# Kernel optimization log

Hardware: AMD Instinct MI355X
Metric: run time of the kernel (lower is better)

Reference implementation:

```python
import jax, jax.numpy as jnp
import numpy as np

B, N, H, L = 8, 256, 128, 3
NF, EF, TD, FH = 6, 15, 4, 64  # node feat, edge feat, temporal dim, flow hidden


def setup_inputs() -> dict:
    key = jax.random.key(0)
    ks = jax.random.split(key, 16)
    s = 0.05
    return {
        "node_features": jax.random.normal(ks[0], (B, N, NF), jnp.float32),
        "edge_features": jax.random.normal(ks[1], (B, N, N, EF), jnp.float32),
        "temporal_features": jax.random.normal(ks[2], (B, N, N, TD), jnp.float32),
        "adjacency": jax.random.randint(ks[3], (N, N), 0, 2, jnp.int32),
        "W_emb": jax.random.normal(ks[4], (NF, H), jnp.float32) * s,
        "b_emb": jnp.zeros((H,), jnp.float32),
        "msg_W": jax.random.normal(ks[5], (L, H + 3, H), jnp.float32) * s,
        "msg_b": jnp.zeros((L, H), jnp.float32),
        "upd_W": jax.random.normal(ks[6], (L, 2 * H, H), jnp.float32) * s,
        "upd_b": jnp.zeros((L, H), jnp.float32),
        "W1": jax.random.normal(ks[7], (2 * H + 3 + TD, FH), jnp.float32) * s,
        "b1": jnp.zeros((FH,), jnp.float32),
        "W2": jax.random.normal(ks[8], (FH, 1), jnp.float32) * s,
        "b2": jnp.zeros((1,), jnp.float32),
    }


def reference(node_features, edge_features, temporal_features, adjacency,
              W_emb, b_emb, msg_W, msg_b, upd_W, upd_b, W1, b1, W2, b2):
    # mask[j, i] = 1 if node i is a neighbor of node j (adjacency[j] > 0)
    mask = (adjacency > 0).astype(node_features.dtype)          # [N, N]
    deg = mask.sum(axis=1)                                      # [N]
    edge_rel = edge_features[..., -3:]                          # [B, N, N, 3]
    # aggregated relation features per destination j: sum_i mask[j,i] * edge_rel[b,i,j,:]
    r_agg = jnp.einsum('ji,bijc->bjc', mask, edge_rel)          # [B, N, 3]

    # node embedding (dropout = identity in eval)
    emb = jax.nn.relu(node_features @ W_emb + b_emb)            # [B, N, H]

    for l in range(L):
        We, Wr = msg_W[l, :H], msg_W[l, H:]                     # [H,H], [3,H]
        # msg_nn is linear, so the masked sum decomposes exactly:
        # messages[b,j] = sum_i mask[j,i]*(emb_i @ We + r_ij @ Wr + b)
        messages = (jnp.einsum('ji,bih->bjh', mask, emb @ We)
                    + r_agg @ Wr
                    + deg[None, :, None] * msg_b[l])            # [B, N, H]
        emb = jax.nn.relu(
            jnp.concatenate([emb, messages], axis=-1) @ upd_W[l] + upd_b[l])

    # pairwise flow MLP, first Linear split by input blocks [emb_i, emb_j, r, t]
    Wi, Wj = W1[:H], W1[H:2 * H]
    Wr1, Wt = W1[2 * H:2 * H + 3], W1[2 * H + 3:]
    hi = emb @ Wi                                               # [B, N, FH]
    hj = emb @ Wj                                               # [B, N, FH]
    h = jax.nn.relu(hi[:, :, None, :] + hj[:, None, :, :]
                    + edge_rel @ Wr1 + temporal_features @ Wt + b1)  # [B,N,N,FH]
    flows = jax.nn.relu(h @ W2 + b2)[..., 0]                    # [B, N, N]
    return flows
```

## Files before the change

### kernel.cpp

```cpp
#include <hip/hip_runtime.h>

#define B 8
#define N 256
#define H 128
#define NF 6
#define EF 15
#define TD 4
#define FH 64
#define M (B*N)

typedef unsigned short u16;
using short8  = __attribute__((ext_vector_type(8))) short;
using short4v = __attribute__((ext_vector_type(4))) short;
using f32x4   = __attribute__((ext_vector_type(4))) float;

__device__ __forceinline__ u16 f2bf(float x) {
    unsigned u = __float_as_uint(x);
    u += 0x7fffu + ((u >> 16) & 1u);
    return (u16)(u >> 16);
}
__device__ __forceinline__ float bf2f(u16 h) {
    return __uint_as_float(((unsigned)h) << 16);
}

__global__ __launch_bounds__(256) void k_setup(
    const float* __restrict__ edge, const int* __restrict__ adj,
    const float* __restrict__ nf, const float* __restrict__ Wemb,
    const float* __restrict__ bemb,
    const float* __restrict__ msg_W, const float* __restrict__ upd_W,
    const float* __restrict__ W1,
    float* __restrict__ e0p, float* __restrict__ e1p, float* __restrict__ e2p,
    float* __restrict__ rp0, float* __restrict__ rp1, float* __restrict__ rp2,
    float* __restrict__ deg,
    u16* __restrict__ WeTh, u16* __restrict__ WeTl,
    u16* __restrict__ UwTh, u16* __restrict__ UwTl,
    u16* __restrict__ W1Th, u16* __restrict__ W1Tl,
    u16* __restrict__ eRh, u16* __restrict__ eRl,
    u16* __restrict__ eTh, u16* __restrict__ eTl)
{
    __shared__ __align__(16) float smem[3848];
    __shared__ float red[4];
    const int t = threadIdx.x;
    const int blk = blockIdx.x;

    if (blk < 2048) {
        const int i = blk & 255;
        const float* src = edge + (size_t)blk * (N * EF);
        float4* s4 = (float4*)smem;
#pragma unroll
        for (int u = 0; u < 4; ++u) {
            int idx = t + u * 256;
            if (idx < (N * EF) / 4) s4[idx] = *(const float4*)(src + idx * 4);
        }
        __syncthreads();
        const int j = t;
        float e0 = smem[j * EF + 12];
        float e1 = smem[j * EF + 13];
        float e2 = smem[j * EF + 14];
        size_t base = (size_t)blk * N + j;
        e0p[base] = e0; e1p[base] = e1; e2p[base] = e2;
        float m = (adj[j * N + i] > 0) ? 1.f : 0.f;
        rp0[base] = m * e0; rp1[base] = m * e1; rp2[base] = m * e2;
    } else if (blk < 2688) {
        int idx = (blk - 2048) * 256 + t;
        float v; u16 *dh, *dl; int d;
        if (idx < 3 * 16384) {
            int l = idx / 16384, r = idx & 16383;
            int c = r >> 7, h = r & 127;
            v = msg_W[l * ((H + 3) * H) + h * H + c];
            dh = WeTh; dl = WeTl; d = idx;
        } else if (idx < 3 * 16384 + 3 * 32768) {
            int r0 = idx - 3 * 16384;
            int l = r0 / 32768, r = r0 & 32767;
            int c = r >> 8, k = r & 255;
            v = upd_W[l * (2 * H * H) + k * H + c];
            dh = UwTh; dl = UwTl; d = r0;
        } else {
            int r0 = idx - 3 * 16384 - 3 * 32768;
            int f = r0 >> 8, k = r0 & 255;
            v = W1[k * FH + f];
            dh = W1Th; dl = W1Tl; d = r0;
        }
        u16 h = f2bf(v);
        dh[d] = h;
        dl[d] = f2bf(v - bf2f(h));
    } else if (blk < 2816) {
        int tile = blk - 2688;
        float (*sout)[132] = (float(*)[132])smem;
        {
            int row = t >> 4, h0 = (t & 15) * 8;
            int gr = tile * 16 + row;
            float xv[NF];
#pragma unroll
            for (int k = 0; k < NF; ++k) xv[k] = nf[gr * NF + k];
#pragma unroll
            for (int c = 0; c < 8; ++c) {
                float a = bemb[h0 + c];
#pragma unroll
                for (int k = 0; k < NF; ++k) a += xv[k] * Wemb[k * H + h0 + c];
                sout[row][h0 + c] = fmaxf(a, 0.f);
            }
        }
        __syncthreads();
        {
            int row = t >> 4, h0 = (t & 15) * 8;
            int gr = tile * 16 + row;
            short8 ph, pl;
#pragma unroll
            for (int c = 0; c < 8; ++c) {
                float x = sout[row][h0 + c];
                u16 h = f2bf(x);
                ph[c] = (short)h;
                pl[c] = (short)f2bf(x - bf2f(h));
            }
            *(short8*)&eRh[(size_t)gr * H + h0] = ph;
            *(short8*)&eRl[(size_t)gr * H + h0] = pl;
        }
        {
            int hh = t >> 1, jj = (t & 1) * 8;
            short8 th, tl;
#pragma unroll
            for (int r = 0; r < 8; ++r) {
                float x = sout[jj + r][hh];
                u16 h = f2bf(x);
                th[r] = (short)h;
                tl[r] = (short)f2bf(x - bf2f(h));
            }
            size_t o = (size_t)(tile >> 4) * H * N + (size_t)hh * N + ((tile & 15) * 16) + jj;
            *(short8*)&eTh[o] = th;
            *(short8*)&eTl[o] = tl;
        }
    } else {
        int jr = blk - 2816;
        float v = (adj[jr * N + t] > 0) ? 1.f : 0.f;
        for (int o = 32; o > 0; o >>= 1) v += __shfl_down(v, o);
        if ((t & 63) == 0) red[t >> 6] = v;
        __syncthreads();
        if (t == 0) deg[jr] = red[0] + red[1] + red[2] + red[3];
    }
}

#define PIPE(NC, LD, COMP)                          \
    LD(0, pA0, pA1);                                \
    LD(1, pB0, pB1);                                \
    WRX(0, pA0, pA1);                               \
    __syncthreads();                                \
    _Pragma("unroll")                               \
    for (int c = 0; c < (NC); c += 2) {             \
        WRX(1, pB0, pB1);                           \
        if (c + 2 < (NC)) LD(c + 2, pA0, pA1);      \
        COMP(c, 0);                                 \
        __syncthreads();                            \
        if (c + 2 < (NC)) WRX(0, pA0, pA1);         \
        if (c + 3 < (NC)) LD(c + 3, pB0, pB1);      \
        COMP(c + 1, 1);                             \
        __syncthreads();                            \
    }

template <bool FIRST, bool LAST>
__global__ __launch_bounds__(512) void k_layer(
    const u16* __restrict__ embR_hi, const u16* __restrict__ embR_lo,
    const u16* __restrict__ embT_hi, const u16* __restrict__ embT_lo,
    const int* __restrict__ adj,
    const float* __restrict__ rp0, const float* __restrict__ rp1,
    const float* __restrict__ rp2, float* __restrict__ ragg,
    const float* __restrict__ deg,
    const u16* __restrict__ WeT_hi, const u16* __restrict__ WeT_lo,
    const float* __restrict__ mwl, const float* __restrict__ mbl,
    const u16* __restrict__ UwT_hi, const u16* __restrict__ UwT_lo,
    const float* __restrict__ ubl,
    u16* __restrict__ oR_hi, u16* __restrict__ oR_lo,
    u16* __restrict__ oT_hi, u16* __restrict__ oT_lo,
    const u16* __restrict__ W1T_hi, const u16* __restrict__ W1T_lo,
    float* __restrict__ hi_out, float* __restrict__ hj_out)
{
    __shared__ __align__(16) u16 sbt[2][2][128][40];
    __shared__ __align__(16) u16 smask[16][264];
    __shared__ __align__(16) u16 semb_hi[16][136], semb_lo[16][136];
    __shared__ __align__(16) u16 sagg_hi[16][136], sagg_lo[16][136];
    __shared__ __align__(16) u16 smsg_hi[16][136], smsg_lo[16][136];
    __shared__ __align__(16) float sout[16][132];
    __shared__ float sragg[16][4];

    const int t = threadIdx.x;
    const int wave = t >> 6, lane = t & 63;
    const int lrow = lane & 15;
    const int kg8  = (lane >> 4) * 8;
    const int rb   = (lane >> 4) * 4;
    const int cb   = wave * 16;
    const int blk  = blockIdx.x;
    const int b    = blk >> 4, tile = blk & 15;
    const int j0   = tile * 16;
    const int gb   = b * N;

    const int sp = t >> 8, task = t & 255;
    const int sh = task >> 2, sseg = (task & 3) * 8;

    short8 pA0, pA1, pB0, pB1;

    {
        int j = t >> 5, i0 = (t & 31) * 8;
        int4 a0 = *(const int4*)(adj + (j0 + j) * N + i0);
        int4 a1 = *(const int4*)(adj + (j0 + j) * N + i0 + 4);
        short8 mrow;
        mrow[0] = (a0.x > 0) ? (short)0x3F80 : (short)0;
        mrow[1] = (a0.y > 0) ? (short)0x3F80 : (short)0;
        mrow[2] = (a0.z > 0) ? (short)0x3F80 : (short)0;
        mrow[3] = (a0.w > 0) ? (short)0x3F80 : (short)0;
        mrow[4] = (a1.x > 0) ? (short)0x3F80 : (short)0;
        mrow[5] = (a1.y > 0) ? (short)0x3F80 : (short)0;
        mrow[6] = (a1.z > 0) ? (short)0x3F80 : (short)0;
        mrow[7] = (a1.w > 0) ? (short)0x3F80 : (short)0;
        *(short8*)&smask[j][i0] = mrow;
        int h0 = (t & 31) * 4;
        *(short4v*)&semb_hi[j][h0] = *(const short4v*)&embR_hi[(size_t)(gb + j0 + j) * H + h0];
        *(short4v*)&semb_lo[j][h0] = *(const short4v*)&embR_lo[(size_t)(gb + j0 + j) * H + h0];
    }

    if constexpr (FIRST) {
        int j16 = t >> 5, ic = t & 31;
        int gj = gb + j0 + j16;
        float s0 = 0.f, s1 = 0.f, s2 = 0.f;
#pragma unroll
        for (int k = 0; k < 8; ++k) {
            size_t o = ((size_t)(gb + ic * 8 + k)) * N + (j0 + j16);
            s0 += rp0[o]; s1 += rp1[o]; s2 += rp2[o];
        }
        for (int o = 16; o > 0; o >>= 1) {
            s0 += __shfl_down(s0, o, 32);
            s1 += __shfl_down(s1, o, 32);
            s2 += __shfl_down(s2, o, 32);
        }
        if (ic == 0) {
            sragg[j16][0] = s0; sragg[j16][1] = s1; sragg[j16][2] = s2;
            float* rg = ragg + (size_t)gj * 3;
            rg[0] = s0; rg[1] = s1; rg[2] = s2;
        }
    } else {
        if (t < 48) sragg[t / 3][t % 3] = ragg[(size_t)(gb + j0 + t / 3) * 3 + (t % 3)];
    }

    const u16* sA_hi = embT_hi + (size_t)b * H * N;
    const u16* sA_lo = embT_lo + (size_t)b * H * N;

#define WRX(buf, q0, q1)                              \
    { *(short8*)&sbt[buf][sp][sh][sseg] = q0;         \
      *(short8*)&sbt[buf][sp][sh + 64][sseg] = q1; }

#define LDA(c, q0, q1)                                                        \
    { const u16* s_ = sp ? sA_lo : sA_hi;                                     \
      q0 = *(const short8*)(s_ + (size_t)sh * N + (c) * 32 + sseg);           \
      q1 = *(const short8*)(s_ + (size_t)(sh + 64) * N + (c) * 32 + sseg); }

#define LDB(c, q0, q1)                                                        \
    { const u16* s_ = sp ? WeT_lo : WeT_hi;                                   \
      q0 = *(const short8*)(s_ + (size_t)sh * H + (c) * 32 + sseg);           \
      q1 = *(const short8*)(s_ + (size_t)(sh + 64) * H + (c) * 32 + sseg); }

#define LDC(c, q0, q1)                                                        \
    { const u16* s_ = sp ? UwT_lo : UwT_hi;                                   \
      q0 = *(const short8*)(s_ + (size_t)sh * 2 * H + (c) * 32 + sseg);       \
      q1 = *(const short8*)(s_ + (size_t)(sh + 64) * 2 * H + (c) * 32 + sseg); }

#define LDD(c, q0, q1)                                                        \
    { const u16* s_ = sp ? W1T_lo : W1T_hi;                                   \
      q0 = *(const short8*)(s_ + (size_t)sh * 256 + (c) * 32 + sseg);         \
      q1 = *(const short8*)(s_ + (size_t)sh * 256 + 128 + (c) * 32 + sseg); }

#define COMPA(c, buf)                                                           \
    { short8 am = *(const short8*)&smask[lrow][(c) * 32 + kg8];                 \
      short8 bh = *(const short8*)&sbt[buf][0][cb + lrow][kg8];                 \
      short8 bl = *(const short8*)&sbt[buf][1][cb + lrow][kg8];                 \
      acc = __builtin_amdgcn_mfma_f32_16x16x32_bf16(am, bh, acc, 0, 0, 0);      \
      acc = __builtin_amdgcn_mfma_f32_16x16x32_bf16(am, bl, acc, 0, 0, 0); }

#define COMPB(c, buf)                                                           \
    { short8 ah = *(const short8*)&sagg_hi[lrow][(c) * 32 + kg8];               \
      short8 al = *(const short8*)&sagg_lo[lrow][(c) * 32 + kg8];               \
      short8 bh = *(const short8*)&sbt[buf][0][cb + lrow][kg8];                 \
      short8 bl = *(const short8*)&sbt[buf][1][cb + lrow][kg8];                 \
      acc = __builtin_amdgcn_mfma_f32_16x16x32_bf16(ah, bh, acc, 0, 0, 0);      \
      acc = __builtin_amdgcn_mfma_f32_16x16x32_bf16(ah, bl, acc, 0, 0, 0);      \
      acc = __builtin_amdgcn_mfma_f32_16x16x32_bf16(al, bh, acc, 0, 0, 0); }

#define COMPC(c, buf)                                                           \
    { int kc = ((c) & 3) * 32 + kg8; short8 ah, al;                             \
      if ((c) < 4) { ah = *(const short8*)&semb_hi[lrow][kc];                   \
                     al = *(const short8*)&semb_lo[lrow][kc]; }                 \
      else         { ah = *(const short8*)&smsg_hi[lrow][kc];                   \
                     al = *(const short8*)&smsg_lo[lrow][kc]; }                 \
      short8 bh = *(const short8*)&sbt[buf][0][cb + lrow][kg8];                 \
      short8 bl = *(const short8*)&sbt[buf][1][cb + lrow][kg8];                 \
      acc = __builtin_amdgcn_mfma_f32_16x16x32_bf16(ah, bh, acc, 0, 0, 0);      \
      acc = __builtin_amdgcn_mfma_f32_16x16x32_bf16(ah, bl, acc, 0, 0, 0);      \
      acc = __builtin_amdgcn_mfma_f32_16x16x32_bf16(al, bh, acc, 0, 0, 0); }

#define COMPD(c, buf)                                                           \
    { short8 ah = *(const short8*)&sagg_hi[lrow][(c) * 32 + kg8];               \
      short8 al = *(const short8*)&sagg_lo[lrow][(c) * 32 + kg8];               \
      short8 bh = *(const short8*)&sbt[buf][0][br][kg8];                        \
      short8 bl = *(const short8*)&sbt[buf][1][br][kg8];                        \
      acc = __builtin_amdgcn_mfma_f32_16x16x32_bf16(ah, bh, acc, 0, 0, 0);      \
      acc = __builtin_amdgcn_mfma_f32_16x16x32_bf16(ah, bl, acc, 0, 0, 0);      \
      acc = __builtin_amdgcn_mfma_f32_16x16x32_bf16(al, bh, acc, 0, 0, 0); }

    f32x4 acc = {0.f, 0.f, 0.f, 0.f};
    PIPE(8, LDA, COMPA)
#pragma unroll
    for (int r = 0; r < 4; ++r) {
        float v = acc[r];
        u16 h = f2bf(v);
        sagg_hi[rb + r][cb + lrow] = h;
        sagg_lo[rb + r][cb + lrow] = f2bf(v - bf2f(h));
    }

    acc = (f32x4){0.f, 0.f, 0.f, 0.f};
    PIPE(4, LDB, COMPB)
    {
        int hp = cb + lrow;
        float w0 = mwl[(H + 0) * H + hp];
        float w1 = mwl[(H + 1) * H + hp];
        float w2 = mwl[(H + 2) * H + hp];
        float mb = mbl[hp];
#pragma unroll
        for (int r = 0; r < 4; ++r) {
            int jl = j0 + rb + r;
            float v = acc[r] + deg[jl] * mb
                    + sragg[rb + r][0] * w0 + sragg[rb + r][1] * w1
                    + sragg[rb + r][2] * w2;
            u16 h = f2bf(v);
            smsg_hi[rb + r][hp] = h;
            smsg_lo[rb + r][hp] = f2bf(v - bf2f(h));
        }
    }

    acc = (f32x4){0.f, 0.f, 0.f, 0.f};
    PIPE(8, LDC, COMPC)
    {
        float ub = ubl[cb + lrow];
#pragma unroll
        for (int r = 0; r < 4; ++r) {
            float v = fmaxf(acc[r] + ub, 0.f);
            if constexpr (LAST) {
                u16 h = f2bf(v);
                sagg_hi[rb + r][cb + lrow] = h;
                sagg_lo[rb + r][cb + lrow] = f2bf(v - bf2f(h));
            } else {
                sout[rb + r][cb + lrow] = v;
            }
        }
    }
    __syncthreads();

    if constexpr (!LAST) {
        {
            int row = t >> 5, h0 = (t & 31) * 4;
            int gr = gb + j0 + row;
            float4 v = *(const float4*)&sout[row][h0];
            float xs[4] = {v.x, v.y, v.z, v.w};
            short4v ph, pl;
#pragma unroll
            for (int c = 0; c < 4; ++c) {
                u16 h = f2bf(xs[c]);
                ph[c] = (short)h;
                pl[c] = (short)f2bf(xs[c] - bf2f(h));
            }
            *(short4v*)&oR_hi[(size_t)gr * H + h0] = ph;
            *(short4v*)&oR_lo[(size_t)gr * H + h0] = pl;
        }
        {
            int hh = t >> 2, jj = (t & 3) * 4;
            short4v th, tl;
#pragma unroll
            for (int r = 0; r < 4; ++r) {
                float x = sout[jj + r][hh];
                u16 h = f2bf(x);
                th[r] = (short)h;
                tl[r] = (short)f2bf(x - bf2f(h));
            }
            size_t o = (size_t)b * H * N + (size_t)hh * N + j0 + jj;
            *(short4v*)&oT_hi[o] = th;
            *(short4v*)&oT_lo[o] = tl;
        }
    } else {
        const int br = ((wave >= 4) ? 64 : 0) + (wave & 3) * 16 + lrow;
        acc = (f32x4){0.f, 0.f, 0.f, 0.f};
        PIPE(4, LDD, COMPD)
#pragma unroll
        for (int r = 0; r < 4; ++r) sout[rb + r][br] = acc[r];
        __syncthreads();
        int row = t >> 5, c0 = (t & 31) * 4;
        int gr = gb + j0 + row;
        float4 v = *(const float4*)&sout[row][c0];
        if (c0 < 64) *(float4*)&hi_out[(size_t)gr * FH + c0] = v;
        else         *(float4*)&hj_out[(size_t)gr * FH + (c0 - 64)] = v;
    }
#undef WRX
#undef LDA
#undef LDB
#undef LDC
#undef LDD
#undef COMPA
#undef COMPB
#undef COMPC
#undef COMPD
}

__global__ __launch_bounds__(256) void k_final(
    const float* __restrict__ hi, const float* __restrict__ hj,
    const float* __restrict__ e0p, const float* __restrict__ e1p,
    const float* __restrict__ e2p, const float* __restrict__ temporal,
    const float* __restrict__ W1, const float* __restrict__ b1,
    const float* __restrict__ W2, const float* __restrict__ b2,
    float* __restrict__ flows) {
    __shared__ float his[8][FH];
    __shared__ float hjs[32][FH + 2];
    __shared__ float wr0[FH], wr1[FH], wr2[FH];
    __shared__ float wt0[FH], wt1[FH], wt2[FH], wt3[FH], bb[FH], w2s[FH];
    int blk = blockIdx.x;
    int jt = blk & 7, it = (blk >> 3) & 31, b = blk >> 8;
    int tid = threadIdx.x;
#pragma unroll
    for (int u = 0; u < 2; ++u) {
        int idx = u * 256 + tid;
        his[idx >> 6][idx & 63] = hi[((size_t)(b * N) + it * 8 + (idx >> 6)) * FH + (idx & 63)];
    }
#pragma unroll
    for (int u = 0; u < 8; ++u) {
        int idx = u * 256 + tid;
        hjs[idx >> 6][idx & 63] = hj[((size_t)(b * N) + jt * 32 + (idx >> 6)) * FH + (idx & 63)];
    }
    {
        int f = tid & 63, g = tid >> 6;
        if (g == 0) { wr0[f] = W1[(2 * H + 0) * FH + f]; wt0[f] = W1[(2 * H + 3) * FH + f]; bb[f] = b1[f]; }
        if (g == 1) { wr1[f] = W1[(2 * H + 1) * FH + f]; wt1[f] = W1[(2 * H + 4) * FH + f]; w2s[f] = W2[f]; }
        if (g == 2) { wr2[f] = W1[(2 * H + 2) * FH + f]; wt2[f] = W1[(2 * H + 5) * FH + f]; }
        if (g == 3) { wt3[f] = W1[(2 * H + 6) * FH + f]; }
    }
    __syncthreads();
    int ti = tid >> 5, tj = tid & 31;
    int i = it * 8 + ti, j = jt * 32 + tj;
    size_t pij = ((size_t)(b * N) + i) * N + j;
    float e0 = e0p[pij], e1 = e1p[pij], e2 = e2p[pij];
    float4 tf = *(const float4*)(temporal + pij * TD);
    float acc = 0.f;
#pragma unroll 8
    for (int f = 0; f < FH; ++f) {
        float v = his[ti][f] + hjs[tj][f] + bb[f]
                + e0 * wr0[f] + e1 * wr1[f] + e2 * wr2[f]
                + tf.x * wt0[f] + tf.y * wt1[f] + tf.z * wt2[f] + tf.w * wt3[f];
        acc += fmaxf(v, 0.f) * w2s[f];
    }
    flows[pij] = fmaxf(acc + b2[0], 0.f);
}

extern "C" void kernel_launch(void* const* d_in, const int* in_sizes, int n_in,
                              void* d_out, int out_size, void* d_ws, size_t ws_size,
                              hipStream_t stream) {
    const float* nf       = (const float*)d_in[0];
    const float* edge     = (const float*)d_in[1];
    const float* temporal = (const float*)d_in[2];
    const int*   adj      = (const int*)d_in[3];
    const float* W_emb    = (const float*)d_in[4];
    const float* b_emb    = (const float*)d_in[5];
    const float* msg_W    = (const float*)d_in[6];
    const float* msg_b    = (const float*)d_in[7];
    const float* upd_W    = (const float*)d_in[8];
    const float* upd_b    = (const float*)d_in[9];
    const float* W1       = (const float*)d_in[10];
    const float* b1       = (const float*)d_in[11];
    const float* W2       = (const float*)d_in[12];
    const float* b2       = (const float*)d_in[13];
    float* out = (float*)d_out;
    (void)in_sizes; (void)n_in; (void)out_size; (void)ws_size;

    char* p = (char*)d_ws;
    auto take = [&](size_t bytes) { char* r = p; p += (bytes + 255) & ~(size_t)255; return r; };
    float* deg   = (float*)take(256 * 4);
    float* ragg  = (float*)take((size_t)M * 3 * 4);
    float* e0p   = (float*)take((size_t)B * N * N * 4);
    float* e1p   = (float*)take((size_t)B * N * N * 4);
    float* e2p   = (float*)take((size_t)B * N * N * 4);
    float* rp0   = (float*)take((size_t)B * N * N * 4);
    float* rp1   = (float*)take((size_t)B * N * N * 4);
    float* rp2   = (float*)take((size_t)B * N * N * 4);
    float* hi    = (float*)take((size_t)M * FH * 4);
    float* hj    = (float*)take((size_t)M * FH * 4);
    u16* eRhA = (u16*)take((size_t)M * H * 2);
    u16* eRlA = (u16*)take((size_t)M * H * 2);
    u16* eThA = (u16*)take((size_t)M * H * 2);
    u16* eTlA = (u16*)take((size_t)M * H * 2);
    u16* eRhB = (u16*)take((size_t)M * H * 2);
    u16* eRlB = (u16*)take((size_t)M * H * 2);
    u16* eThB = (u16*)take((size_t)M * H * 2);
    u16* eTlB = (u16*)take((size_t)M * H * 2);
    u16* WeTh = (u16*)take(3 * 16384 * 2);
    u16* WeTl = (u16*)take(3 * 16384 * 2);
    u16* UwTh = (u16*)take(3 * 32768 * 2);
    u16* UwTl = (u16*)take(3 * 32768 * 2);
    u16* W1Th = (u16*)take(16384 * 2);
    u16* W1Tl = (u16*)take(16384 * 2);

    k_setup<<<3072, 256, 0, stream>>>(edge, adj, nf, W_emb, b_emb,
                                      msg_W, upd_W, W1,
                                      e0p, e1p, e2p, rp0, rp1, rp2, deg,
                                      WeTh, WeTl, UwTh, UwTl, W1Th, W1Tl,
                                      eRhA, eRlA, eThA, eTlA);

    const int mwS = (H + 3) * H;
    k_layer<true, false><<<128, 512, 0, stream>>>(
        eRhA, eRlA, eThA, eTlA, adj, rp0, rp1, rp2, ragg, deg,
        WeTh + 0 * 16384, WeTl + 0 * 16384, msg_W + 0 * mwS, msg_b + 0 * H,
        UwTh + 0 * 32768, UwTl + 0 * 32768, upd_b + 0 * H,
        eRhB, eRlB, eThB, eTlB, W1Th, W1Tl, hi, hj);
    k_layer<false, false><<<128, 512, 0, stream>>>(
        eRhB, eRlB, eThB, eTlB, adj, rp0, rp1, rp2, ragg, deg,
        WeTh + 1 * 16384, WeTl + 1 * 16384, msg_W + 1 * mwS, msg_b + 1 * H,
        UwTh + 1 * 32768, UwTl + 1 * 32768, upd_b + 1 * H,
        eRhA, eRlA, eThA, eTlA, W1Th, W1Tl, hi, hj);
    k_layer<false, true><<<128, 512, 0, stream>>>(
        eRhA, eRlA, eThA, eTlA, adj, rp0, rp1, rp2, ragg, deg,
        WeTh + 2 * 16384, WeTl + 2 * 16384, msg_W + 2 * mwS, msg_b + 2 * H,
        UwTh + 2 * 32768, UwTl + 2 * 32768, upd_b + 2 * H,
        eRhB, eRlB, eThB, eTlB, W1Th, W1Tl, hi, hj);

    k_final<<<2048, 256, 0, stream>>>(hi, hj, e0p, e1p, e2p, temporal,
                                      W1, b1, W2, b2, out);
}
```

Baseline: 73.78 us.

## Fuse setup, layers and flow MLP into one cooperative persistent kernel

Replaces the five separate launches (setup, three GNN layers, final flow MLP) with a single cooperative kernel of 256 blocks that separates the phases with grid-wide syncs and overlays their shared memory in a union. The setup phase is rebalanced so each block streams eight edge rows with double-buffered loads, and the final phase loops over four j-tiles per block. The aim is to remove launch gaps and tail effects between short kernels. In exchange, only 128 of 256 blocks do work in the layer phases, grid syncs add their own cost, and occupancy is bounded by the union's shared memory size.

```diff
diff --git a/kernel.cpp b/kernel.cpp
--- a/kernel.cpp
+++ b/kernel.cpp
@@ -1,4 +1,7 @@
 #include <hip/hip_runtime.h>
+#include <hip/hip_cooperative_groups.h>
+
+namespace cg = cooperative_groups;
 
 #define B 8
 #define N 256
@@ -23,121 +26,59 @@
     return __uint_as_float(((unsigned)h) << 16);
 }
 
-__global__ __launch_bounds__(256) void k_setup(
-    const float* __restrict__ edge, const int* __restrict__ adj,
-    const float* __restrict__ nf, const float* __restrict__ Wemb,
-    const float* __restrict__ bemb,
-    const float* __restrict__ msg_W, const float* __restrict__ upd_W,
-    const float* __restrict__ W1,
-    float* __restrict__ e0p, float* __restrict__ e1p, float* __restrict__ e2p,
-    float* __restrict__ rp0, float* __restrict__ rp1, float* __restrict__ rp2,
-    float* __restrict__ deg,
-    u16* __restrict__ WeTh, u16* __restrict__ WeTl,
-    u16* __restrict__ UwTh, u16* __restrict__ UwTl,
-    u16* __restrict__ W1Th, u16* __restrict__ W1Tl,
-    u16* __restrict__ eRh, u16* __restrict__ eRl,
-    u16* __restrict__ eTh, u16* __restrict__ eTl)
-{
-    __shared__ __align__(16) float smem[3848];
-    __shared__ float red[4];
-    const int t = threadIdx.x;
-    const int blk = blockIdx.x;
-
-    if (blk < 2048) {
-        const int i = blk & 255;
-        const float* src = edge + (size_t)blk * (N * EF);
-        float4* s4 = (float4*)smem;
-#pragma unroll
-        for (int u = 0; u < 4; ++u) {
-            int idx = t + u * 256;
-            if (idx < (N * EF) / 4) s4[idx] = *(const float4*)(src + idx * 4);
-        }
-        __syncthreads();
-        const int j = t;
-        float e0 = smem[j * EF + 12];
-        float e1 = smem[j * EF + 13];
-        float e2 = smem[j * EF + 14];
-        size_t base = (size_t)blk * N + j;
-        e0p[base] = e0; e1p[base] = e1; e2p[base] = e2;
-        float m = (adj[j * N + i] > 0) ? 1.f : 0.f;
-        rp0[base] = m * e0; rp1[base] = m * e1; rp2[base] = m * e2;
-    } else if (blk < 2688) {
-        int idx = (blk - 2048) * 256 + t;
-        float v; u16 *dh, *dl; int d;
-        if (idx < 3 * 16384) {
-            int l = idx / 16384, r = idx & 16383;
-            int c = r >> 7, h = r & 127;
-            v = msg_W[l * ((H + 3) * H) + h * H + c];
-            dh = WeTh; dl = WeTl; d = idx;
-        } else if (idx < 3 * 16384 + 3 * 32768) {
-            int r0 = idx - 3 * 16384;
-            int l = r0 / 32768, r = r0 & 32767;
-            int c = r >> 8, k = r & 255;
-            v = upd_W[l * (2 * H * H) + k * H + c];
-            dh = UwTh; dl = UwTl; d = r0;
-        } else {
-            int r0 = idx - 3 * 16384 - 3 * 32768;
-            int f = r0 >> 8, k = r0 & 255;
-            v = W1[k * FH + f];
-            dh = W1Th; dl = W1Tl; d = r0;
-        }
-        u16 h = f2bf(v);
-        dh[d] = h;
-        dl[d] = f2bf(v - bf2f(h));
-    } else if (blk < 2816) {
-        int tile = blk - 2688;
-        float (*sout)[132] = (float(*)[132])smem;
-        {
-            int row = t >> 4, h0 = (t & 15) * 8;
-            int gr = tile * 16 + row;
-            float xv[NF];
-#pragma unroll
-            for (int k = 0; k < NF; ++k) xv[k] = nf[gr * NF + k];
-#pragma unroll
-            for (int c = 0; c < 8; ++c) {
-                float a = bemb[h0 + c];
-#pragma unroll
-                for (int k = 0; k < NF; ++k) a += xv[k] * Wemb[k * H + h0 + c];
-                sout[row][h0 + c] = fmaxf(a, 0.f);
-            }
-        }
-        __syncthreads();
-        {
-            int row = t >> 4, h0 = (t & 15) * 8;
-            int gr = tile * 16 + row;
-            short8 ph, pl;
-#pragma unroll
-            for (int c = 0; c < 8; ++c) {
-                float x = sout[row][h0 + c];
-                u16 h = f2bf(x);
-                ph[c] = (short)h;
-                pl[c] = (short)f2bf(x - bf2f(h));
-            }
-            *(short8*)&eRh[(size_t)gr * H + h0] = ph;
-            *(short8*)&eRl[(size_t)gr * H + h0] = pl;
-        }
-        {
-            int hh = t >> 1, jj = (t & 1) * 8;
-            short8 th, tl;
-#pragma unroll
-            for (int r = 0; r < 8; ++r) {
-                float x = sout[jj + r][hh];
-                u16 h = f2bf(x);
-                th[r] = (short)h;
-                tl[r] = (short)f2bf(x - bf2f(h));
-            }
-            size_t o = (size_t)(tile >> 4) * H * N + (size_t)hh * N + ((tile & 15) * 16) + jj;
-            *(short8*)&eTh[o] = th;
-            *(short8*)&eTl[o] = tl;
-        }
+struct LayerSM {
+    u16 sbt[2][2][128][40];
+    u16 smask[16][264];
+    u16 semb_hi[16][136], semb_lo[16][136];
+    u16 sagg_hi[16][136], sagg_lo[16][136];
+    u16 smsg_hi[16][136], smsg_lo[16][136];
+    float sout[16][132];
+    float sragg[16][4];
+};
+struct SetupSM {
+    float edge[2][3840];
+    float sout[16][132];
+    float red[8];
+};
+struct FinalSM {
+    float his[8][FH];
+    float hjs[64][FH + 3];
+    float wr[3][FH], wt[4][FH], bb[FH], w2s[FH];
+};
+union SMu { LayerSM L; SetupSM S; FinalSM F; };
+
+struct Params {
+    const float* edge; const float* temporal; const int* adj;
+    const float* nf; const float* Wemb; const float* bemb;
+    const float* msgW; const float* msgb; const float* updW; const float* updb;
+    const float* W1; const float* b1; const float* W2; const float* b2;
+    float *e0p, *e1p, *e2p, *rp0, *rp1, *rp2, *deg, *ragg, *hi, *hj, *out;
+    u16 *eRhA, *eRlA, *eThA, *eTlA, *eRhB, *eRlB, *eThB, *eTlB;
+    u16 *WeTh, *WeTl, *UwTh, *UwTl, *W1Th, *W1Tl;
+};
+
+__device__ __forceinline__ void wtrans(int idx, const Params& p) {
+    float v; u16 *dh, *dl; int d;
+    if (idx < 3 * 16384) {
+        int l = idx / 16384, r = idx & 16383;
+        int c = r >> 7, h = r & 127;
+        v = p.msgW[l * ((H + 3) * H) + h * H + c];
+        dh = p.WeTh; dl = p.WeTl; d = idx;
+    } else if (idx < 3 * 16384 + 3 * 32768) {
+        int r0 = idx - 3 * 16384;
+        int l = r0 / 32768, r = r0 & 32767;
+        int c = r >> 8, k = r & 255;
+        v = p.updW[l * (2 * H * H) + k * H + c];
+        dh = p.UwTh; dl = p.UwTl; d = r0;
     } else {
-        int jr = blk - 2816;
-        float v = (adj[jr * N + t] > 0) ? 1.f : 0.f;
-        for (int o = 32; o > 0; o >>= 1) v += __shfl_down(v, o);
-        if ((t & 63) == 0) red[t >> 6] = v;
-        __syncthreads();
-        if (t == 0) deg[jr] = red[0] + red[1] + red[2] + red[3];
-    }
+        int r0 = idx - 3 * 16384 - 3 * 32768;
+        int f = r0 >> 8, k = r0 & 255;
+        v = p.W1[k * FH + f];
+        dh = p.W1Th; dl = p.W1Tl; d = r0;
+    }
+    u16 h = f2bf(v);
+    dh[d] = h;
+    dl[d] = f2bf(v - bf2f(h));
 }
 
 #define PIPE(NC, LD, COMP)                          \
@@ -158,41 +99,28 @@
     }
 
 template <bool FIRST, bool LAST>
-__global__ __launch_bounds__(512) void k_layer(
-    const u16* __restrict__ embR_hi, const u16* __restrict__ embR_lo,
-    const u16* __restrict__ embT_hi, const u16* __restrict__ embT_lo,
-    const int* __restrict__ adj,
-    const float* __restrict__ rp0, const float* __restrict__ rp1,
-    const float* __restrict__ rp2, float* __restrict__ ragg,
-    const float* __restrict__ deg,
-    const u16* __restrict__ WeT_hi, const u16* __restrict__ WeT_lo,
-    const float* __restrict__ mwl, const float* __restrict__ mbl,
-    const u16* __restrict__ UwT_hi, const u16* __restrict__ UwT_lo,
-    const float* __restrict__ ubl,
-    u16* __restrict__ oR_hi, u16* __restrict__ oR_lo,
-    u16* __restrict__ oT_hi, u16* __restrict__ oT_lo,
-    const u16* __restrict__ W1T_hi, const u16* __restrict__ W1T_lo,
-    float* __restrict__ hi_out, float* __restrict__ hj_out)
+__device__ void layer_body(SMu& sm, const Params& p, int blk, int t,
+    const u16* embR_hi, const u16* embR_lo,
+    const u16* embT_hi, const u16* embT_lo,
+    const u16* WeT_hi, const u16* WeT_lo,
+    const float* mwl, const float* mbl,
+    const u16* UwT_hi, const u16* UwT_lo, const float* ubl,
+    u16* oR_hi, u16* oR_lo, u16* oT_hi, u16* oT_lo)
 {
-    __shared__ __align__(16) u16 sbt[2][2][128][40];
-    __shared__ __align__(16) u16 smask[16][264];
-    __shared__ __align__(16) u16 semb_hi[16][136], semb_lo[16][136];
-    __shared__ __align__(16) u16 sagg_hi[16][136], sagg_lo[16][136];
-    __shared__ __align__(16) u16 smsg_hi[16][136], smsg_lo[16][136];
-    __shared__ __align__(16) float sout[16][132];
-    __shared__ float sragg[16][4];
-
-    const int t = threadIdx.x;
+    auto& sbt = sm.L.sbt;       auto& smask = sm.L.smask;
+    auto& semb_hi = sm.L.semb_hi; auto& semb_lo = sm.L.semb_lo;
+    auto& sagg_hi = sm.L.sagg_hi; auto& sagg_lo = sm.L.sagg_lo;
+    auto& smsg_hi = sm.L.smsg_hi; auto& smsg_lo = sm.L.smsg_lo;
+    auto& sout = sm.L.sout;     auto& sragg = sm.L.sragg;
+
     const int wave = t >> 6, lane = t & 63;
     const int lrow = lane & 15;
     const int kg8  = (lane >> 4) * 8;
     const int rb   = (lane >> 4) * 4;
     const int cb   = wave * 16;
-    const int blk  = blockIdx.x;
     const int b    = blk >> 4, tile = blk & 15;
     const int j0   = tile * 16;
     const int gb   = b * N;
-
     const int sp = t >> 8, task = t & 255;
     const int sh = task >> 2, sseg = (task & 3) * 8;
 
@@ -200,8 +128,8 @@
 
     {
         int j = t >> 5, i0 = (t & 31) * 8;
-        int4 a0 = *(const int4*)(adj + (j0 + j) * N + i0);
-        int4 a1 = *(const int4*)(adj + (j0 + j) * N + i0 + 4);
+        int4 a0 = *(const int4*)(p.adj + (j0 + j) * N + i0);
+        int4 a1 = *(const int4*)(p.adj + (j0 + j) * N + i0 + 4);
         short8 mrow;
         mrow[0] = (a0.x > 0) ? (short)0x3F80 : (short)0;
         mrow[1] = (a0.y > 0) ? (short)0x3F80 : (short)0;
@@ -224,7 +152,7 @@
 #pragma unroll
         for (int k = 0; k < 8; ++k) {
             size_t o = ((size_t)(gb + ic * 8 + k)) * N + (j0 + j16);
-            s0 += rp0[o]; s1 += rp1[o]; s2 += rp2[o];
+            s0 += p.rp0[o]; s1 += p.rp1[o]; s2 += p.rp2[o];
         }
         for (int o = 16; o > 0; o >>= 1) {
             s0 += __shfl_down(s0, o, 32);
@@ -233,11 +161,11 @@
         }
         if (ic == 0) {
             sragg[j16][0] = s0; sragg[j16][1] = s1; sragg[j16][2] = s2;
-            float* rg = ragg + (size_t)gj * 3;
+            float* rg = p.ragg + (size_t)gj * 3;
             rg[0] = s0; rg[1] = s1; rg[2] = s2;
         }
     } else {
-        if (t < 48) sragg[t / 3][t % 3] = ragg[(size_t)(gb + j0 + t / 3) * 3 + (t % 3)];
+        if (t < 48) sragg[t / 3][t % 3] = p.ragg[(size_t)(gb + j0 + t / 3) * 3 + (t % 3)];
     }
 
     const u16* sA_hi = embT_hi + (size_t)b * H * N;
@@ -263,7 +191,7 @@
       q1 = *(const short8*)(s_ + (size_t)(sh + 64) * 2 * H + (c) * 32 + sseg); }
 
 #define LDD(c, q0, q1)                                                        \
-    { const u16* s_ = sp ? W1T_lo : W1T_hi;                                   \
+    { const u16* s_ = sp ? p.W1Tl : p.W1Th;                                   \
       q0 = *(const short8*)(s_ + (size_t)sh * 256 + (c) * 32 + sseg);         \
       q1 = *(const short8*)(s_ + (size_t)sh * 256 + 128 + (c) * 32 + sseg); }
 
@@ -325,7 +253,7 @@
 #pragma unroll
         for (int r = 0; r < 4; ++r) {
             int jl = j0 + rb + r;
-            float v = acc[r] + deg[jl] * mb
+            float v = acc[r] + p.deg[jl] * mb
                     + sragg[rb + r][0] * w0 + sragg[rb + r][1] * w1
                     + sragg[rb + r][2] * w2;
             u16 h = f2bf(v);
@@ -392,8 +320,8 @@
         int row = t >> 5, c0 = (t & 31) * 4;
         int gr = gb + j0 + row;
         float4 v = *(const float4*)&sout[row][c0];
-        if (c0 < 64) *(float4*)&hi_out[(size_t)gr * FH + c0] = v;
-        else         *(float4*)&hj_out[(size_t)gr * FH + (c0 - 64)] = v;
+        if (c0 < 64) *(float4*)&p.hi[(size_t)gr * FH + c0] = v;
+        else         *(float4*)&p.hj[(size_t)gr * FH + (c0 - 64)] = v;
     }
 #undef WRX
 #undef LDA
@@ -406,124 +334,221 @@
 #undef COMPD
 }
 
-__global__ __launch_bounds__(256) void k_final(
-    const float* __restrict__ hi, const float* __restrict__ hj,
-    const float* __restrict__ e0p, const float* __restrict__ e1p,
-    const float* __restrict__ e2p, const float* __restrict__ temporal,
-    const float* __restrict__ W1, const float* __restrict__ b1,
-    const float* __restrict__ W2, const float* __restrict__ b2,
-    float* __restrict__ flows) {
-    __shared__ float his[8][FH];
-    __shared__ float hjs[32][FH + 2];
-    __shared__ float wr0[FH], wr1[FH], wr2[FH];
-    __shared__ float wt0[FH], wt1[FH], wt2[FH], wt3[FH], bb[FH], w2s[FH];
-    int blk = blockIdx.x;
-    int jt = blk & 7, it = (blk >> 3) & 31, b = blk >> 8;
-    int tid = threadIdx.x;
-#pragma unroll
-    for (int u = 0; u < 2; ++u) {
-        int idx = u * 256 + tid;
-        his[idx >> 6][idx & 63] = hi[((size_t)(b * N) + it * 8 + (idx >> 6)) * FH + (idx & 63)];
-    }
-#pragma unroll
-    for (int u = 0; u < 8; ++u) {
-        int idx = u * 256 + tid;
-        hjs[idx >> 6][idx & 63] = hj[((size_t)(b * N) + jt * 32 + (idx >> 6)) * FH + (idx & 63)];
-    }
+__global__ __launch_bounds__(512, 2) void k_mega(Params p) {
+    cg::grid_group grid = cg::this_grid();
+    __shared__ SMu sm;
+    const int blk = blockIdx.x;
+    const int t = threadIdx.x;
+
     {
-        int f = tid & 63, g = tid >> 6;
-        if (g == 0) { wr0[f] = W1[(2 * H + 0) * FH + f]; wt0[f] = W1[(2 * H + 3) * FH + f]; bb[f] = b1[f]; }
-        if (g == 1) { wr1[f] = W1[(2 * H + 1) * FH + f]; wt1[f] = W1[(2 * H + 4) * FH + f]; w2s[f] = W2[f]; }
-        if (g == 2) { wr2[f] = W1[(2 * H + 2) * FH + f]; wt2[f] = W1[(2 * H + 5) * FH + f]; }
-        if (g == 3) { wt3[f] = W1[(2 * H + 6) * FH + f]; }
-    }
-    __syncthreads();
-    int ti = tid >> 5, tj = tid & 31;
-    int i = it * 8 + ti, j = jt * 32 + tj;
-    size_t pij = ((size_t)(b * N) + i) * N + j;
-    float e0 = e0p[pij], e1 = e1p[pij], e2 = e2p[pij];
-    float4 tf = *(const float4*)(temporal + pij * TD);
-    float acc = 0.f;
+        const int b = blk >> 5, ic = blk & 31;
+        float4 r0, r1;
+        auto loadTask = [&](int k) {
+            const float* src = p.edge + ((size_t)(b * N + ic * 8 + k)) * (N * EF);
+            r0 = *(const float4*)(src + t * 4);
+            if (t < 448) r1 = *(const float4*)(src + t * 4 + 2048);
+        };
+        auto writeTask = [&](int buf) {
+            *(float4*)&sm.S.edge[buf][t * 4] = r0;
+            if (t < 448) *(float4*)&sm.S.edge[buf][t * 4 + 2048] = r1;
+        };
+        loadTask(0);
+        writeTask(0);
+        for (int k = 0; k < 8; ++k) {
+            __syncthreads();
+            if (k < 7) loadTask(k + 1);
+            {
+                const int i = ic * 8 + k;
+                const int j = t & 255;
+                const float* eb = sm.S.edge[k & 1];
+                float e0 = eb[j * EF + 12];
+                float e1 = eb[j * EF + 13];
+                float e2 = eb[j * EF + 14];
+                size_t base = ((size_t)(b * N + i)) * N + j;
+                if (t < 256) {
+                    p.e0p[base] = e0; p.e1p[base] = e1; p.e2p[base] = e2;
+                } else {
+                    float m = (p.adj[j * N + i] > 0) ? 1.f : 0.f;
+                    p.rp0[base] = m * e0; p.rp1[base] = m * e1; p.rp2[base] = m * e2;
+                }
+            }
+            if (k < 7) writeTask((k + 1) & 1);
+        }
+        __syncthreads();
+
+        wtrans(blk * 512 + t, p);
+        if (blk < 64) wtrans(131072 + blk * 512 + t, p);
+
+        if (blk < 128) {
+            const int tile = blk;
+            int row = t >> 5, h0 = (t & 31) * 4;
+            int gr = tile * 16 + row;
+            float xv[NF];
+#pragma unroll
+            for (int k = 0; k < NF; ++k) xv[k] = p.nf[gr * NF + k];
+#pragma unroll
+            for (int c = 0; c < 4; ++c) {
+                float a = p.bemb[h0 + c];
+#pragma unroll
+                for (int k = 0; k < NF; ++k) a += xv[k] * p.Wemb[k * H + h0 + c];
+                sm.S.sout[row][h0 + c] = fmaxf(a, 0.f);
+            }
+            __syncthreads();
+            {
+                short4v ph, pl;
+#pragma unroll
+                for (int c = 0; c < 4; ++c) {
+                    float x = sm.S.sout[row][h0 + c];
+                    u16 h = f2bf(x);
+                    ph[c] = (short)h;
+                    pl[c] = (short)f2bf(x - bf2f(h));
+                }
+                *(short4v*)&p.eRhA[(size_t)gr * H + h0] = ph;
+                *(short4v*)&p.eRlA[(size_t)gr * H + h0] = pl;
+            }
+            {
+                int hh = t >> 2, jj = (t & 3) * 4;
+                short4v th, tl;
+#pragma unroll
+                for (int r = 0; r < 4; ++r) {
+                    float x = sm.S.sout[jj + r][hh];
+                    u16 h = f2bf(x);
+                    th[r] = (short)h;
+                    tl[r] = (short)f2bf(x - bf2f(h));
+                }
+                size_t o = (size_t)(tile >> 4) * H * N + (size_t)hh * N + ((tile & 15) * 16) + jj;
+                *(short4v*)&p.eThA[o] = th;
+                *(short4v*)&p.eTlA[o] = tl;
+            }
+        }
+
+        {
+            float v = 0.f;
+            if (t < 256) v = (p.adj[blk * N + t] > 0) ? 1.f : 0.f;
+            for (int o = 32; o > 0; o >>= 1) v += __shfl_down(v, o);
+            if ((t & 63) == 0) sm.S.red[t >> 6] = v;
+            __syncthreads();
+            if (t == 0) p.deg[blk] = sm.S.red[0] + sm.S.red[1] + sm.S.red[2] + sm.S.red[3];
+        }
+    }
+    grid.sync();
+
+    const int mwS = (H + 3) * H;
+    if (blk < 128)
+        layer_body<true, false>(sm, p, blk, t,
+            p.eRhA, p.eRlA, p.eThA, p.eTlA,
+            p.WeTh + 0 * 16384, p.WeTl + 0 * 16384, p.msgW + 0 * mwS, p.msgb + 0 * H,
+            p.UwTh + 0 * 32768, p.UwTl + 0 * 32768, p.updb + 0 * H,
+            p.eRhB, p.eRlB, p.eThB, p.eTlB);
+    grid.sync();
+    if (blk < 128)
+        layer_body<false, false>(sm, p, blk, t,
+            p.eRhB, p.eRlB, p.eThB, p.eTlB,
+            p.WeTh + 1 * 16384, p.WeTl + 1 * 16384, p.msgW + 1 * mwS, p.msgb + 1 * H,
+            p.UwTh + 1 * 32768, p.UwTl + 1 * 32768, p.updb + 1 * H,
+            p.eRhA, p.eRlA, p.eThA, p.eTlA);
+    grid.sync();
+    if (blk < 128)
+        layer_body<false, true>(sm, p, blk, t,
+            p.eRhA, p.eRlA, p.eThA, p.eTlA,
+            p.WeTh + 2 * 16384, p.WeTl + 2 * 16384, p.msgW + 2 * mwS, p.msgb + 2 * H,
+            p.UwTh + 2 * 32768, p.UwTl + 2 * 32768, p.updb + 2 * H,
+            p.eRhB, p.eRlB, p.eThB, p.eTlB);
+    grid.sync();
+
+    {
+        FinalSM& F = sm.F;
+        const int b = blk >> 5, it = blk & 31;
+        {
+            int f = t & 63, g = t >> 6;
+            if (g == 0) F.wr[0][f] = p.W1[(2 * H + 0) * FH + f];
+            if (g == 1) F.wr[1][f] = p.W1[(2 * H + 1) * FH + f];
+            if (g == 2) F.wr[2][f] = p.W1[(2 * H + 2) * FH + f];
+            if (g == 3) F.wt[0][f] = p.W1[(2 * H + 3) * FH + f];
+            if (g == 4) F.wt[1][f] = p.W1[(2 * H + 4) * FH + f];
+            if (g == 5) F.wt[2][f] = p.W1[(2 * H + 5) * FH + f];
+            if (g == 6) F.wt[3][f] = p.W1[(2 * H + 6) * FH + f];
+            if (g == 7) { F.bb[f] = p.b1[f]; F.w2s[f] = p.W2[f]; }
+        }
+        F.his[t >> 6][t & 63] = p.hi[((size_t)(b * N) + it * 8 + (t >> 6)) * FH + (t & 63)];
+        const float b2v = p.b2[0];
+        for (int jp = 0; jp < 4; ++jp) {
+#pragma unroll
+            for (int u = 0; u < 8; ++u) {
+                int idx = u * 512 + t;
+                int r = idx >> 6, c = idx & 63;
+                F.hjs[r][c] = p.hj[((size_t)(b * N) + jp * 64 + r) * FH + c];
+            }
+            __syncthreads();
+            int ti = t >> 6, tj = t & 63;
+            int i = it * 8 + ti, j = jp * 64 + tj;
+            size_t pij = ((size_t)(b * N) + i) * N + j;
+            float e0 = p.e0p[pij], e1 = p.e1p[pij], e2 = p.e2p[pij];
+            float4 tf = *(const float4*)(p.temporal + pij * TD);
+            float acc = 0.f;
 #pragma unroll 8
-    for (int f = 0; f < FH; ++f) {
-        float v = his[ti][f] + hjs[tj][f] + bb[f]
-                + e0 * wr0[f] + e1 * wr1[f] + e2 * wr2[f]
-                + tf.x * wt0[f] + tf.y * wt1[f] + tf.z * wt2[f] + tf.w * wt3[f];
-        acc += fmaxf(v, 0.f) * w2s[f];
-    }
-    flows[pij] = fmaxf(acc + b2[0], 0.f);
+            for (int ff = 0; ff < FH; ++ff) {
+                float v = F.his[ti][ff] + F.hjs[tj][ff] + F.bb[ff]
+                        + e0 * F.wr[0][ff] + e1 * F.wr[1][ff] + e2 * F.wr[2][ff]
+                        + tf.x * F.wt[0][ff] + tf.y * F.wt[1][ff]
+                        + tf.z * F.wt[2][ff] + tf.w * F.wt[3][ff];
+                acc += fmaxf(v, 0.f) * F.w2s[ff];
+            }
+            p.out[pij] = fmaxf(acc + b2v, 0.f);
+            __syncthreads();
+        }
+    }
 }
 
 extern "C" void kernel_launch(void* const* d_in, const int* in_sizes, int n_in,
                               void* d_out, int out_size, void* d_ws, size_t ws_size,
                               hipStream_t stream) {
-    const float* nf       = (const float*)d_in[0];
-    const float* edge     = (const float*)d_in[1];
-    const float* temporal = (const float*)d_in[2];
-    const int*   adj      = (const int*)d_in[3];
-    const float* W_emb    = (const float*)d_in[4];
-    const float* b_emb    = (const float*)d_in[5];
-    const float* msg_W    = (const float*)d_in[6];
-    const float* msg_b    = (const float*)d_in[7];
-    const float* upd_W    = (const float*)d_in[8];
-    const float* upd_b    = (const float*)d_in[9];
-    const float* W1       = (const float*)d_in[10];
-    const float* b1       = (const float*)d_in[11];
-    const float* W2       = (const float*)d_in[12];
-    const float* b2       = (const float*)d_in[13];
-    float* out = (float*)d_out;
     (void)in_sizes; (void)n_in; (void)out_size; (void)ws_size;
-
-    char* p = (char*)d_ws;
-    auto take = [&](size_t bytes) { char* r = p; p += (bytes + 255) & ~(size_t)255; return r; };
-    float* deg   = (float*)take(256 * 4);
-    float* ragg  = (float*)take((size_t)M * 3 * 4);
-    float* e0p   = (float*)take((size_t)B * N * N * 4);
-    float* e1p   = (float*)take((size_t)B * N * N * 4);
-    float* e2p   = (float*)take((size_t)B * N * N * 4);
-    float* rp0   = (float*)take((size_t)B * N * N * 4);
-    float* rp1   = (float*)take((size_t)B * N * N * 4);
-    float* rp2   = (float*)take((size_t)B * N * N * 4);
-    float* hi    = (float*)take((size_t)M * FH * 4);
-    float* hj    = (float*)take((size_t)M * FH * 4);
-    u16* eRhA = (u16*)take((size_t)M * H * 2);
-    u16* eRlA = (u16*)take((size_t)M * H * 2);
-    u16* eThA = (u16*)take((size_t)M * H * 2);
-    u16* eTlA = (u16*)take((size_t)M * H * 2);
-    u16* eRhB = (u16*)take((size_t)M * H * 2);
-    u16* eRlB = (u16*)take((size_t)M * H * 2);
-    u16* eThB = (u16*)take((size_t)M * H * 2);
-    u16* eTlB = (u16*)take((size_t)M * H * 2);
-    u16* WeTh = (u16*)take(3 * 16384 * 2);
-    u16* WeTl = (u16*)take(3 * 16384 * 2);
-    u16* UwTh = (u16*)take(3 * 32768 * 2);
-    u16* UwTl = (u16*)take(3 * 32768 * 2);
-    u16* W1Th = (u16*)take(16384 * 2);
-    u16* W1Tl = (u16*)take(16384 * 2);
-
-    k_setup<<<3072, 256, 0, stream>>>(edge, adj, nf, W_emb, b_emb,
-                                      msg_W, upd_W, W1,
-                                      e0p, e1p, e2p, rp0, rp1, rp2, deg,
-                                      WeTh, WeTl, UwTh, UwTl, W1Th, W1Tl,
-                                      eRhA, eRlA, eThA, eTlA);
-
-    const int mwS = (H + 3) * H;
-    k_layer<true, false><<<128, 512, 0, stream>>>(
-        eRhA, eRlA, eThA, eTlA, adj, rp0, rp1, rp2, ragg, deg,
-        WeTh + 0 * 16384, WeTl + 0 * 16384, msg_W + 0 * mwS, msg_b + 0 * H,
-        UwTh + 0 * 32768, UwTl + 0 * 32768, upd_b + 0 * H,
-        eRhB, eRlB, eThB, eTlB, W1Th, W1Tl, hi, hj);
-    k_layer<false, false><<<128, 512, 0, stream>>>(
-        eRhB, eRlB, eThB, eTlB, adj, rp0, rp1, rp2, ragg, deg,
-        WeTh + 1 * 16384, WeTl + 1 * 16384, msg_W + 1 * mwS, msg_b + 1 * H,
-        UwTh + 1 * 32768, UwTl + 1 * 32768, upd_b + 1 * H,
-        eRhA, eRlA, eThA, eTlA, W1Th, W1Tl, hi, hj);
-    k_layer<false, true><<<128, 512, 0, stream>>>(
-        eRhA, eRlA, eThA, eTlA, adj, rp0, rp1, rp2, ragg, deg,
-        WeTh + 2 * 16384, WeTl + 2 * 16384, msg_W + 2 * mwS, msg_b + 2 * H,
-        UwTh + 2 * 32768, UwTl + 2 * 32768, upd_b + 2 * H,
-        eRhB, eRlB, eThB, eTlB, W1Th, W1Tl, hi, hj);
-
-    k_final<<<2048, 256, 0, stream>>>(hi, hj, e0p, e1p, e2p, temporal,
-                                      W1, b1, W2, b2, out);
+    Params hp;
+    hp.nf       = (const float*)d_in[0];
+    hp.edge     = (const float*)d_in[1];
+    hp.temporal = (const float*)d_in[2];
+    hp.adj      = (const int*)d_in[3];
+    hp.Wemb     = (const float*)d_in[4];
+    hp.bemb     = (const float*)d_in[5];
+    hp.msgW     = (const float*)d_in[6];
+    hp.msgb     = (const float*)d_in[7];
+    hp.updW     = (const float*)d_in[8];
+    hp.updb     = (const float*)d_in[9];
+    hp.W1       = (const float*)d_in[10];
+    hp.b1       = (const float*)d_in[11];
+    hp.W2       = (const float*)d_in[12];
+    hp.b2       = (const float*)d_in[13];
+    hp.out      = (float*)d_out;
+
+    char* ptr = (char*)d_ws;
+    auto take = [&](size_t bytes) { char* r = ptr; ptr += (bytes + 255) & ~(size_t)255; return r; };
+    hp.deg  = (float*)take(256 * 4);
+    hp.ragg = (float*)take((size_t)M * 3 * 4);
+    hp.e0p  = (float*)take((size_t)B * N * N * 4);
+    hp.e1p  = (float*)take((size_t)B * N * N * 4);
+    hp.e2p  = (float*)take((size_t)B * N * N * 4);
+    hp.rp0  = (float*)take((size_t)B * N * N * 4);
+    hp.rp1  = (float*)take((size_t)B * N * N * 4);
+    hp.rp2  = (float*)take((size_t)B * N * N * 4);
+    hp.hi   = (float*)take((size_t)M * FH * 4);
+    hp.hj   = (float*)take((size_t)M * FH * 4);
+    hp.eRhA = (u16*)take((size_t)M * H * 2);
+    hp.eRlA = (u16*)take((size_t)M * H * 2);
+    hp.eThA = (u16*)take((size_t)M * H * 2);
+    hp.eTlA = (u16*)take((size_t)M * H * 2);
+    hp.eRhB = (u16*)take((size_t)M * H * 2);
+    hp.eRlB = (u16*)take((size_t)M * H * 2);
+    hp.eThB = (u16*)take((size_t)M * H * 2);
+    hp.eTlB = (u16*)take((size_t)M * H * 2);
+    hp.WeTh = (u16*)take(3 * 16384 * 2);
+    hp.WeTl = (u16*)take(3 * 16384 * 2);
+    hp.UwTh = (u16*)take(3 * 32768 * 2);
+    hp.UwTl = (u16*)take(3 * 32768 * 2);
+    hp.W1Th = (u16*)take(16384 * 2);
+    hp.W1Tl = (u16*)take(16384 * 2);
+
+    void* kargs[] = { (void*)&hp };
+    hipLaunchCooperativeKernel((const void*)k_mega, dim3(256), dim3(512),
+                               kargs, 0, stream);
 }
```

Measured after the change: 214.2 us. 2.9x slower.
